# Performance work log

Measured on AMD Instinct MI355X. Metric: run time of the kernel, lower is better.

## Reference

```python
import jax, jax.numpy as jnp
import numpy as np

TEMPERATURE = 0.07
NEG_INF = jnp.float32(-2**32 + 1)


def setup_inputs() -> dict:
    key = jax.random.key(0)
    k1, k2, k3, k4, k5 = jax.random.split(key, 5)
    N, Na, d_in, d_out, n_rel = 10000, 10000, 256, 64, 3
    x = jax.random.normal(k1, (N, d_out), dtype=jnp.float32) * 0.1
    anchor = jax.random.normal(k2, (Na, d_in), dtype=jnp.float32) * 0.1
    # xavier-uniform-like scale for wt [d_in, d_out]
    lim = float(np.sqrt(6.0 / (d_in + d_out)))
    wt = jax.random.uniform(k3, (d_in, d_out), dtype=jnp.float32, minval=-lim, maxval=lim)
    weight = jax.random.normal(k4, (n_rel,), dtype=jnp.float32)
    # sparse adjacency (materialized dense as the original does via .to_dense())
    adjs = jax.random.bernoulli(k5, 0.01, (n_rel, Na, N))
    return {"x": x, "weight": weight, "adjs": adjs, "idx": 0, "anchor": anchor, "wt": wt}


def reference(x, weight, adjs, idx, anchor, wt):
    # x: [N, d_out], anchor: [Na, d_in], wt: [d_in, d_out], adjs: [n_rel, Na, N] bool
    adj = adjs[idx]                                   # [Na, N]
    scores = (anchor @ wt) @ x.T                      # [Na, N]
    masked = jnp.where(adj, scores, NEG_INF)          # adjacency mask
    atten = jax.nn.softmax(masked / TEMPERATURE, axis=1)
    output = atten @ x                                # [Na, d_out]
    return weight[idx] * output
```

## Files before the change

### kernel.cpp

```cpp
#include <hip/hip_runtime.h>

#define NN    10000
#define NA    10000
#define DIN   256
#define DOUT  64
#define INV_T (1.0f / 0.07f)
#define CAP   1024

typedef unsigned int uv4 __attribute__((ext_vector_type(4)));


__global__ __launch_bounds__(256) void attn_kernel(
    const float* __restrict__ x,
    const float* __restrict__ weight,
    const unsigned int* __restrict__ adjs,
    const int*   __restrict__ idxp,
    const float* __restrict__ anchor,
    const float* __restrict__ wt,
    float* __restrict__ out)
{
    __shared__ float arow[DIN];
    __shared__ float pr[DOUT];
    __shared__ int   jl[CAP];
    __shared__ float ps[CAP];
    __shared__ float red[256];
    __shared__ float wred[8];
    __shared__ int   cnt;

    const int t    = threadIdx.x;
    const int row  = blockIdx.x;
    const int w    = t >> 6;
    const int lane = t & 63;

    if (t < 64) ((float4*)arow)[t] =
        ((const float4*)(anchor + (size_t)row * DIN))[t];
    if (t == 0) cnt = 0;
    __syncthreads();

    const int idx = idxp[0];

    {
        const uv4* ar = (const uv4*)(adjs + ((size_t)idx * NA + row) * NN);
        uv4 v[10];
#pragma unroll
        for (int it = 0; it < 10; ++it) {
            const int cch = t + 256 * it;
            uv4 vv = {0u, 0u, 0u, 0u};
            if (cch < NN / 4) vv = __builtin_nontemporal_load(ar + cch);
            v[it] = vv;
        }
        unsigned long long hm = 0ull;
#pragma unroll
        for (int it = 0; it < 10; ++it) {
            unsigned int nz = (v[it].x ? 1u : 0u) | (v[it].y ? 2u : 0u) |
                              (v[it].z ? 4u : 0u) | (v[it].w ? 8u : 0u);
            hm |= (unsigned long long)nz << (it * 4);
        }
        const int mycnt = __popcll(hm);
        int base = 0;
        if (mycnt) base = atomicAdd(&cnt, mycnt);
        while (hm) {
            const int b = __ffsll((long long)hm) - 1;
            hm &= hm - 1;
            const int it = b >> 2, ww = b & 3;
            if (base < CAP) jl[base] = (t + 256 * it) * 4 + ww;
            ++base;
        }
    }

    {
        const int seg = t >> 6, c = t & 63;
        float acc = 0.f;
        const int k0 = seg * 64;
#pragma unroll 8
        for (int k = k0; k < k0 + 64; ++k)
            acc = fmaf(arow[k], wt[k * DOUT + c], acc);
        red[t] = acc;
    }
    __syncthreads();

    if (t < DOUT) pr[t] = red[t] + red[64 + t] + red[128 + t] + red[192 + t];
    int nc = cnt; if (nc > CAP) nc = CAP;
    __syncthreads();

    if (nc == 0) {
        if (t < DOUT) out[(size_t)row * DOUT + t] = 0.f;
        return;
    }

    {
        const int g = t >> 4, l = t & 15;
        const float4 pv = ((const float4*)pr)[l];
        for (int s = g; s < nc; s += 16) {
            const int j = jl[s];
            float4 xv = ((const float4*)(x + (size_t)j * DOUT))[l];
            float d = xv.x * pv.x + xv.y * pv.y + xv.z * pv.z + xv.w * pv.w;
            d += __shfl_xor(d, 1);
            d += __shfl_xor(d, 2);
            d += __shfl_xor(d, 4);
            d += __shfl_xor(d, 8);
            if (l == 0) ps[s] = d * INV_T;
        }
    }
    __syncthreads();

    float lm = -3.4e38f;
    for (int s = t; s < nc; s += 256) lm = fmaxf(lm, ps[s]);
#pragma unroll
    for (int o = 32; o > 0; o >>= 1) lm = fmaxf(lm, __shfl_xor(lm, o));
    if (lane == 0) wred[w] = lm;
    __syncthreads();
    const float m = fmaxf(fmaxf(wred[0], wred[1]), fmaxf(wred[2], wred[3]));

    float lsum = 0.f;
    for (int s = t; s < nc; s += 256) {
        float p = __expf(ps[s] - m);
        ps[s] = p;
        lsum += p;
    }
#pragma unroll
    for (int o = 32; o > 0; o >>= 1) lsum += __shfl_xor(lsum, o);
    if (lane == 0) wred[4 + w] = lsum;
    __syncthreads();
    const float scale = weight[idx] /
        (wred[4] + wred[5] + wred[6] + wred[7]);

    {
        const int c = t & 63, seg = t >> 6;
        float acc = 0.f;
        for (int s = seg; s < nc; s += 4)
            acc = fmaf(ps[s], x[(size_t)jl[s] * DOUT + c], acc);
        red[t] = acc;
        __syncthreads();
        if (t < DOUT) {
            float o = (red[t] + red[64 + t] + red[128 + t] + red[192 + t]) * scale;
            __builtin_nontemporal_store(o, out + (size_t)row * DOUT + t);
        }
    }
}

extern "C" void kernel_launch(void* const* d_in, const int* in_sizes, int n_in,
                              void* d_out, int out_size, void* d_ws, size_t ws_size,
                              hipStream_t stream) {
    const float*        x      = (const float*)d_in[0];
    const float*        weight = (const float*)d_in[1];
    const unsigned int* adjs   = (const unsigned int*)d_in[2];
    const int*          idxp   = (const int*)d_in[3];
    const float*        anchor = (const float*)d_in[4];
    const float*        wt     = (const float*)d_in[5];
    float*              out    = (float*)d_out;

    attn_kernel<<<NA, 256, 0, stream>>>(x, weight, adjs, idxp, anchor, wt, out);
}
```

Before: 1.377 ms.

## Split adjacency scan and attention into two kernels via workspace index lists

Splits the fused kernel in two. The first kernel streams the dense adjacency mask and compacts each row's nonzero column indices into a workspace list. The second kernel reads those lists and does the projection, softmax and gather. The per-row capacity drops from 1024 to 192 entries, which shrinks shared memory and may allow more concurrent blocks. The split adds a round trip through global memory for the index lists and an extra kernel launch, and rows with more than 192 neighbors would be silently truncated.

```diff
diff --git a/kernel.cpp b/kernel.cpp
--- a/kernel.cpp
+++ b/kernel.cpp
@@ -5,10 +5,160 @@
 #define DIN   256
 #define DOUT  64
 #define INV_T (1.0f / 0.07f)
+#define CAPW  192
 #define CAP   1024
 
 typedef unsigned int uv4 __attribute__((ext_vector_type(4)));
 
+
+__global__ __launch_bounds__(256) void scan_kernel(
+    const unsigned int* __restrict__ adjs,
+    const int*          __restrict__ idxp,
+    int*                __restrict__ wcnt,
+    int*                __restrict__ wlist)
+{
+    __shared__ int jl[CAPW];
+    __shared__ int cnt;
+
+    const int t   = threadIdx.x;
+    const int row = blockIdx.x;
+    if (t == 0) cnt = 0;
+    __syncthreads();
+
+    const int idx = idxp[0];
+    const uv4* ar = (const uv4*)(adjs + ((size_t)idx * NA + row) * NN);
+
+    uv4 v[10];
+#pragma unroll
+    for (int it = 0; it < 10; ++it) {
+        const int cch = t + 256 * it;
+        uv4 vv = {0u, 0u, 0u, 0u};
+        if (cch < NN / 4) vv = ar[cch];
+        v[it] = vv;
+    }
+    unsigned long long hm = 0ull;
+#pragma unroll
+    for (int it = 0; it < 10; ++it) {
+        unsigned int nz = (v[it].x ? 1u : 0u) | (v[it].y ? 2u : 0u) |
+                          (v[it].z ? 4u : 0u) | (v[it].w ? 8u : 0u);
+        hm |= (unsigned long long)nz << (it * 4);
+    }
+    const int mycnt = __popcll(hm);
+    int base = 0;
+    if (mycnt) base = atomicAdd(&cnt, mycnt);
+    while (hm) {
+        const int b = __ffsll((long long)hm) - 1;
+        hm &= hm - 1;
+        const int it = b >> 2, ww = b & 3;
+        if (base < CAPW) jl[base] = (t + 256 * it) * 4 + ww;
+        ++base;
+    }
+    __syncthreads();
+
+    int nc = cnt; if (nc > CAPW) nc = CAPW;
+    if (t == 0) wcnt[row] = nc;
+    for (int s = t; s < nc; s += 256) wlist[(size_t)row * CAPW + s] = jl[s];
+}
+
+__global__ __launch_bounds__(256) void attn2_kernel(
+    const float* __restrict__ x,
+    const float* __restrict__ weight,
+    const int*   __restrict__ idxp,
+    const float* __restrict__ anchor,
+    const float* __restrict__ wt,
+    const int*   __restrict__ wcnt,
+    const int*   __restrict__ wlist,
+    float* __restrict__ out)
+{
+    __shared__ float arow[DIN];
+    __shared__ float pr[DOUT];
+    __shared__ int   jl[CAPW];
+    __shared__ float ps[CAPW];
+    __shared__ float red[256];
+    __shared__ float wred[8];
+
+    const int t    = threadIdx.x;
+    const int row  = blockIdx.x;
+    const int w    = t >> 6;
+    const int lane = t & 63;
+
+    if (t < 64) ((float4*)arow)[t] =
+        ((const float4*)(anchor + (size_t)row * DIN))[t];
+    __syncthreads();
+
+    const int idx = idxp[0];
+    const int nc  = wcnt[row];
+    for (int s = t; s < nc; s += 256) jl[s] = wlist[(size_t)row * CAPW + s];
+
+    {
+        const int seg = t >> 6, c = t & 63;
+        float acc = 0.f;
+        const int k0 = seg * 64;
+#pragma unroll 8
+        for (int k = k0; k < k0 + 64; ++k)
+            acc = fmaf(arow[k], wt[k * DOUT + c], acc);
+        red[t] = acc;
+    }
+    __syncthreads();
+
+    if (t < DOUT) pr[t] = red[t] + red[64 + t] + red[128 + t] + red[192 + t];
+    __syncthreads();
+
+    if (nc == 0) {
+        if (t < DOUT) out[(size_t)row * DOUT + t] = 0.f;
+        return;
+    }
+
+    {
+        const int g = t >> 4, l = t & 15;
+        const float4 pv = ((const float4*)pr)[l];
+        for (int s = g; s < nc; s += 16) {
+            const int j = jl[s];
+            float4 xv = ((const float4*)(x + (size_t)j * DOUT))[l];
+            float d = xv.x * pv.x + xv.y * pv.y + xv.z * pv.z + xv.w * pv.w;
+            d += __shfl_xor(d, 1);
+            d += __shfl_xor(d, 2);
+            d += __shfl_xor(d, 4);
+            d += __shfl_xor(d, 8);
+            if (l == 0) ps[s] = d * INV_T;
+        }
+    }
+    __syncthreads();
+
+    float lm = -3.4e38f;
+    for (int s = t; s < nc; s += 256) lm = fmaxf(lm, ps[s]);
+#pragma unroll
+    for (int o = 32; o > 0; o >>= 1) lm = fmaxf(lm, __shfl_xor(lm, o));
+    if (lane == 0) wred[w] = lm;
+    __syncthreads();
+    const float m = fmaxf(fmaxf(wred[0], wred[1]), fmaxf(wred[2], wred[3]));
+
+    float lsum = 0.f;
+    for (int s = t; s < nc; s += 256) {
+        float p = __expf(ps[s] - m);
+        ps[s] = p;
+        lsum += p;
+    }
+#pragma unroll
+    for (int o = 32; o > 0; o >>= 1) lsum += __shfl_xor(lsum, o);
+    if (lane == 0) wred[4 + w] = lsum;
+    __syncthreads();
+    const float scale = weight[idx] /
+        (wred[4] + wred[5] + wred[6] + wred[7]);
+
+    {
+        const int c = t & 63, seg = t >> 6;
+        float acc = 0.f;
+        for (int s = seg; s < nc; s += 4)
+            acc = fmaf(ps[s], x[(size_t)jl[s] * DOUT + c], acc);
+        red[t] = acc;
+        __syncthreads();
+        if (t < DOUT) {
+            float o = (red[t] + red[64 + t] + red[128 + t] + red[192 + t]) * scale;
+            __builtin_nontemporal_store(o, out + (size_t)row * DOUT + t);
+        }
+    }
+}
 
 __global__ __launch_bounds__(256) void attn_kernel(
     const float* __restrict__ x,
@@ -150,5 +300,14 @@
     const float*        wt     = (const float*)d_in[5];
     float*              out    = (float*)d_out;
 
-    attn_kernel<<<NA, 256, 0, stream>>>(x, weight, adjs, idxp, anchor, wt, out);
+    const size_t need = sizeof(int) * ((size_t)NA + (size_t)NA * CAPW);
+    if (d_ws && ws_size >= need) {
+        int* wcnt  = (int*)d_ws;
+        int* wlist = wcnt + NA;
+        scan_kernel<<<NA, 256, 0, stream>>>(adjs, idxp, wcnt, wlist);
+        attn2_kernel<<<NA, 256, 0, stream>>>(x, weight, idxp, anchor, wt,
+                                             wcnt, wlist, out);
+    } else {
+        attn_kernel<<<NA, 256, 0, stream>>>(x, weight, adjs, idxp, anchor, wt, out);
+    }
 }
```

After: 1.417 ms. 1.03x slower.
